# Performance work log

Hardware: AMD Instinct MI355X
Metric: run time of the kernel (lower is better)

## Reference

```python
import jax, jax.numpy as jnp
import numpy as np

N_NODES = 50000
N_EDGES = 640000
IN_CH = 128
OUT_CH = 128


def setup_inputs() -> dict:
    key = jax.random.key(0)
    k1, k2, k3, k4 = jax.random.split(key, 4)
    x = jax.random.normal(k1, (N_NODES, IN_CH), dtype=jnp.float32)
    edge_index = jax.random.randint(k2, (2, N_EDGES), 0, N_NODES, dtype=jnp.int32)
    # nn.Linear params: W [out, in], b [out]
    bound = 1.0 / np.sqrt(IN_CH)
    W = jax.random.uniform(k3, (OUT_CH, IN_CH), minval=-bound, maxval=bound, dtype=jnp.float32)
    b = jax.random.uniform(k4, (OUT_CH,), minval=-bound, maxval=bound, dtype=jnp.float32)
    return {"x": x, "edge_index": edge_index, "W": W, "b": b}


def reference(x, edge_index, W, b):
    row, col = edge_index[0], edge_index[1]
    num_nodes = x.shape[0]
    # degree of each destination node (clamped to >= 1)
    deg = jax.ops.segment_sum(jnp.ones(row.shape[0], dtype=x.dtype), row,
                              num_segments=num_nodes)
    deg = jnp.maximum(deg, 1.0)
    # gather neighbor features and scatter-add into destinations
    agg = jax.ops.segment_sum(x[col], row, num_segments=num_nodes)
    agg = agg / deg[:, None]
    # residual + linear
    return (x + agg) @ W.T + b
```

## Files before the change

### kernel.cpp

```cpp
#include <hip/hip_runtime.h>

#define N_NODES 50000
#define N_EDGES 640000
#define CH 128
#define NBINS 1563
#define NTILES 1563
#define FILLB 128
#define EPB 5000
#define OBW (NBINS + 1)
#define CAPR 48

typedef __bf16 bf16_t;
typedef bf16_t bf16x8 __attribute__((ext_vector_type(8)));
typedef float f32x4 __attribute__((ext_vector_type(4)));

__device__ __forceinline__ ushort f2bf(float f) {
  union { float f; unsigned u; } v; v.f = f;
  unsigned r = v.u + 0x7FFFu + ((v.u >> 16) & 1u);
  return (ushort)(r >> 16);
}
__device__ __forceinline__ float bflo(unsigned u) {
  union { unsigned u; float f; } v; v.u = u << 16; return v.f;
}
__device__ __forceinline__ float bfhi(unsigned u) {
  union { unsigned u; float f; } v; v.u = u & 0xFFFF0000u; return v.f;
}
__device__ __forceinline__ unsigned pack2(float lo, float hi) {
  return (unsigned)f2bf(lo) | ((unsigned)f2bf(hi) << 16);
}
__device__ __forceinline__ void addrow(float* acc, uint4 v) {
  acc[0] += bflo(v.x); acc[1] += bfhi(v.x);
  acc[2] += bflo(v.y); acc[3] += bfhi(v.y);
  acc[4] += bflo(v.z); acc[5] += bfhi(v.z);
  acc[6] += bflo(v.w); acc[7] += bfhi(v.w);
}


__global__ __launch_bounds__(256) void fill_conv(const int* __restrict__ row,
                                                 const int* __restrict__ col,
                                                 unsigned* __restrict__ binRec,
                                                 ushort* __restrict__ obo,
                                                 const float4* __restrict__ x4,
                                                 uint4* __restrict__ xb4,
                                                 const float4* __restrict__ W4,
                                                 uint4* __restrict__ Wb4) {
  __shared__ int cnt[NBINS];
  __shared__ int parts[256];
  __shared__ __align__(16) unsigned recbuf[EPB];
  int bid = blockIdx.x;
  int tid = threadIdx.x;
  if (bid < FILLB) {
    for (int i = tid; i < NBINS; i += 256) cnt[i] = 0;
    __syncthreads();
    int base = bid * EPB;
    int4 r4s[5], c4s[5];
    bool val[5];
#pragma unroll
    for (int b = 0; b < 5; ++b) {
      int idx4 = b * 1024 + tid * 4;
      val[b] = idx4 < EPB;
      if (val[b]) {
        r4s[b] = *(const int4*)(row + base + idx4);
        c4s[b] = *(const int4*)(col + base + idx4);
      }
    }
    unsigned pkv[20];
    unsigned colp[10];
#pragma unroll
    for (int b = 0; b < 5; ++b) {
      if (val[b]) {
        int rr[4] = {r4s[b].x, r4s[b].y, r4s[b].z, r4s[b].w};
        int cc[4] = {c4s[b].x, c4s[b].y, c4s[b].z, c4s[b].w};
#pragma unroll
        for (int j = 0; j < 4; ++j) {
          int bi = rr[j] >> 5;
          int rk = atomicAdd(&cnt[bi], 1);
          pkv[b * 4 + j] = ((unsigned)bi << 13) |
                           ((unsigned)(rr[j] & 31) << 8) | (unsigned)rk;
        }
        colp[b * 2]     = ((unsigned)cc[0] & 0xFFFFu) | ((unsigned)cc[1] << 16);
        colp[b * 2 + 1] = ((unsigned)cc[2] & 0xFFFFu) | ((unsigned)cc[3] << 16);
      } else {
#pragma unroll
        for (int j = 0; j < 4; ++j) pkv[b * 4 + j] = 0xFFFFFFFFu;
        colp[b * 2] = 0; colp[b * 2 + 1] = 0;
      }
    }
    __syncthreads();
    int c7[7];
    int s = 0;
#pragma unroll
    for (int k = 0; k < 7; ++k) {
      int i = tid * 7 + k;
      int c = (i < NBINS) ? cnt[i] : 0;
      c7[k] = c; s += c;
    }
    parts[tid] = s;
    __syncthreads();
    for (int off = 1; off < 256; off <<= 1) {
      int v = (tid >= off) ? parts[tid - off] : 0;
      __syncthreads();
      parts[tid] += v;
      __syncthreads();
    }
    int run = (tid > 0) ? parts[tid - 1] : 0;
    ushort* orow = obo + bid * OBW;
#pragma unroll
    for (int k = 0; k < 7; ++k) {
      int i = tid * 7 + k;
      if (i < NBINS) {
        orow[i] = (ushort)run;
        cnt[i] = run;
        run += c7[k];
      }
    }
    if (tid == 0) orow[NBINS] = (ushort)EPB;
    __syncthreads();
#pragma unroll
    for (int k = 0; k < 20; ++k) {
      unsigned p = pkv[k];
      if (p != 0xFFFFFFFFu) {
        int bi = (int)(p >> 13);
        int lr5 = (int)((p >> 8) & 31u);
        int rk = (int)(p & 255u);
        unsigned cw = (colp[k >> 1] >> ((k & 1) * 16)) & 0xFFFFu;
        recbuf[cnt[bi] + rk] = ((unsigned)lr5 << 16) | cw;
      }
    }
    __syncthreads();
    uint4* gb4 = (uint4*)(binRec + base);
    const uint4* rb4 = (const uint4*)recbuf;
    for (int j = tid; j < EPB / 4; j += 256) gb4[j] = rb4[j];
  } else if (bid < FILLB + 3125) {
    int i = (bid - FILLB) * 256 + tid;
    float4 a = x4[i * 2], b = x4[i * 2 + 1];
    uint4 o;
    o.x = pack2(a.x, a.y); o.y = pack2(a.z, a.w);
    o.z = pack2(b.x, b.y); o.w = pack2(b.z, b.w);
    xb4[i] = o;
  } else {
    for (int i = tid; i < 2048; i += 256) {
      float4 c = W4[i * 2], d = W4[i * 2 + 1];
      uint4 w;
      w.x = pack2(c.x, c.y); w.y = pack2(c.z, c.w);
      w.z = pack2(d.x, d.y); w.w = pack2(d.z, d.w);
      Wb4[i] = w;
    }
  }
}

__global__ __launch_bounds__(256) void fused(const uint4* __restrict__ xb4,
                                             const unsigned* __restrict__ binRec,
                                             const ushort* __restrict__ obo,
                                             const uint4* __restrict__ Wb4,
                                             const float4* __restrict__ bias4,
                                             float4* __restrict__ out4) {
  __shared__ ushort hT[32 * CH];
  __shared__ __align__(16) ushort colL[32 * CAPR];
  __shared__ int rowcnt[32];
  int tid = threadIdx.x;
  int g = blockIdx.x;
  int m0 = g * 32;

  if (tid < 32) rowcnt[tid] = 0;
  __syncthreads();
  {
    int i = tid >> 1, sub = tid & 1;
    const ushort* orow = obo + i * OBW + g;
    int o0 = orow[0], o1 = orow[1];
    const unsigned* rbase = binRec + i * EPB;
    for (int p = o0 + sub; p < o1; p += 2) {
      unsigned rec = __builtin_nontemporal_load(rbase + p);
      int lr = (int)(rec >> 16);
      int pp = atomicAdd(&rowcnt[lr], 1);
      if (pp < CAPR) colL[lr * CAPR + pp] = (ushort)(rec & 0xFFFFu);
    }
  }
  __syncthreads();

  int wv = tid >> 6;
  int lane = tid & 63;
  int q = lane & 15;
  int grp = lane >> 4;
#pragma unroll
  for (int t = 0; t < 2; ++t) {
    int r = wv * 8 + t * 4 + grp;
    int node = m0 + r;
    int deg = rowcnt[r];
    int degc = deg < CAPR ? deg : CAPR;
    const ushort* arow = colL + r * CAPR;
    int nc = node < N_NODES ? node : 0;
    uint4 xi = xb4[nc * 16 + q];
    float acc[8] = {0.f, 0.f, 0.f, 0.f, 0.f, 0.f, 0.f, 0.f};
    int e = 0;
    for (; e + 7 < degc; e += 8) {
      uint4 ids = *(const uint4*)(arow + e);
      int n0 = ids.x & 0xFFFF, n1 = ids.x >> 16;
      int n2 = ids.y & 0xFFFF, n3 = ids.y >> 16;
      int n4 = ids.z & 0xFFFF, n5 = ids.z >> 16;
      int n6 = ids.w & 0xFFFF, n7 = ids.w >> 16;
      uint4 v0 = xb4[n0 * 16 + q];
      uint4 v1 = xb4[n1 * 16 + q];
      uint4 v2 = xb4[n2 * 16 + q];
      uint4 v3 = xb4[n3 * 16 + q];
      uint4 v4 = xb4[n4 * 16 + q];
      uint4 v5 = xb4[n5 * 16 + q];
      uint4 v6 = xb4[n6 * 16 + q];
      uint4 v7 = xb4[n7 * 16 + q];
      addrow(acc, v0); addrow(acc, v1); addrow(acc, v2); addrow(acc, v3);
      addrow(acc, v4); addrow(acc, v5); addrow(acc, v6); addrow(acc, v7);
    }
    if (e + 3 < degc) {
      uint2 ids = *(const uint2*)(arow + e);
      int n0 = ids.x & 0xFFFF, n1 = ids.x >> 16;
      int n2 = ids.y & 0xFFFF, n3 = ids.y >> 16;
      uint4 v0 = xb4[n0 * 16 + q];
      uint4 v1 = xb4[n1 * 16 + q];
      uint4 v2 = xb4[n2 * 16 + q];
      uint4 v3 = xb4[n3 * 16 + q];
      addrow(acc, v0); addrow(acc, v1); addrow(acc, v2); addrow(acc, v3);
      e += 4;
    }
    for (; e < degc; ++e) {
      uint4 v = xb4[(int)arow[e] * 16 + q];
      addrow(acc, v);
    }
    uint4 o = make_uint4(0, 0, 0, 0);
    if (node < N_NODES) {
      float s = 1.0f / fmaxf((float)deg, 1.0f);
      o.x = pack2(bflo(xi.x) + acc[0] * s, bfhi(xi.x) + acc[1] * s);
      o.y = pack2(bflo(xi.y) + acc[2] * s, bfhi(xi.y) + acc[3] * s);
      o.z = pack2(bflo(xi.z) + acc[4] * s, bfhi(xi.z) + acc[5] * s);
      o.w = pack2(bflo(xi.w) + acc[6] * s, bfhi(xi.w) + acc[7] * s);
    }
    *(uint4*)&hT[r * CH + ((q ^ (r & 15)) << 3)] = o;
  }
  __syncthreads();

  int qq = grp;
  int mt = wv & 1;
  int nbase = (wv >> 1) * 4;
  const ushort* hbase = &hT[(mt * 16 + q) * CH];
  bf16x8 hb0 = *(const bf16x8*)(hbase + (((qq + 0) ^ q) << 3));
  bf16x8 hb1 = *(const bf16x8*)(hbase + (((qq + 4) ^ q) << 3));
  bf16x8 hb2 = *(const bf16x8*)(hbase + (((qq + 8) ^ q) << 3));
  bf16x8 hb3 = *(const bf16x8*)(hbase + (((qq + 12) ^ q) << 3));
  int m = m0 + mt * 16 + q;
#pragma unroll
  for (int i = 0; i < 4; ++i) {
    int nt = nbase + i;
    const uint4* wr = Wb4 + (nt * 16 + q) * 16 + qq;
    bf16x8 w0 = __builtin_bit_cast(bf16x8, wr[0]);
    bf16x8 w1 = __builtin_bit_cast(bf16x8, wr[4]);
    bf16x8 w2 = __builtin_bit_cast(bf16x8, wr[8]);
    bf16x8 w3 = __builtin_bit_cast(bf16x8, wr[12]);
    f32x4 acc = {0.f, 0.f, 0.f, 0.f};
    acc = __builtin_amdgcn_mfma_f32_16x16x32_bf16(w0, hb0, acc, 0, 0, 0);
    acc = __builtin_amdgcn_mfma_f32_16x16x32_bf16(w1, hb1, acc, 0, 0, 0);
    acc = __builtin_amdgcn_mfma_f32_16x16x32_bf16(w2, hb2, acc, 0, 0, 0);
    acc = __builtin_amdgcn_mfma_f32_16x16x32_bf16(w3, hb3, acc, 0, 0, 0);
    if (m < N_NODES) {
      float4 bv = bias4[nt * 4 + qq];
      f32x4 o;
      o.x = acc[0] + bv.x;
      o.y = acc[1] + bv.y;
      o.z = acc[2] + bv.z;
      o.w = acc[3] + bv.w;
      __builtin_nontemporal_store(o, (f32x4*)(out4 + (size_t)m * 32 + nt * 4 + qq));
    }
  }
}

extern "C" void kernel_launch(void* const* d_in, const int* in_sizes, int n_in,
                              void* d_out, int out_size, void* d_ws, size_t ws_size,
                              hipStream_t stream) {
  const float* x  = (const float*)d_in[0];
  const int*   ei = (const int*)d_in[1];
  const float* W  = (const float*)d_in[2];
  const float* bb = (const float*)d_in[3];

  char* ws = (char*)d_ws;
  unsigned* binRec = (unsigned*)ws;
  ushort*   obo    = (ushort*)(ws + 2560000);
  uint4*    Wb4    = (uint4*)(ws + 2960384);
  uint4*    xb4    = (uint4*)(ws + 2993152);

  fill_conv<<<FILLB + 3125 + 1, 256, 0, stream>>>(ei, ei + N_EDGES, binRec, obo,
                                                  (const float4*)x, xb4,
                                                  (const float4*)W, Wb4);
  fused<<<NTILES, 256, 0, stream>>>(xb4, binRec, obo, Wb4,
                                    (const float4*)bb, (float4*)d_out);
}
```

Baseline: 131.8 us.

## Split binning into 256 blocks with transposed offsets, widen fused kernel to 512 threads

```diff
diff --git a/kernel.cpp b/kernel.cpp
--- a/kernel.cpp
+++ b/kernel.cpp
@@ -5,9 +5,8 @@
 #define CH 128
 #define NBINS 1563
 #define NTILES 1563
-#define FILLB 128
-#define EPB 5000
-#define OBW (NBINS + 1)
+#define BINB 256
+#define EPB 2500
 #define CAPR 48
 
 typedef __bf16 bf16_t;
@@ -36,103 +35,105 @@
 }
 
 
-__global__ __launch_bounds__(256) void fill_conv(const int* __restrict__ row,
-                                                 const int* __restrict__ col,
-                                                 unsigned* __restrict__ binRec,
-                                                 ushort* __restrict__ obo,
-                                                 const float4* __restrict__ x4,
-                                                 uint4* __restrict__ xb4,
-                                                 const float4* __restrict__ W4,
-                                                 uint4* __restrict__ Wb4) {
+__global__ __launch_bounds__(256) void bink(const int* __restrict__ row,
+                                            const int* __restrict__ col,
+                                            unsigned* __restrict__ binRec,
+                                            ushort* __restrict__ obot) {
   __shared__ int cnt[NBINS];
   __shared__ int parts[256];
   __shared__ __align__(16) unsigned recbuf[EPB];
   int bid = blockIdx.x;
   int tid = threadIdx.x;
-  if (bid < FILLB) {
-    for (int i = tid; i < NBINS; i += 256) cnt[i] = 0;
+  for (int i = tid; i < NBINS; i += 256) cnt[i] = 0;
+  __syncthreads();
+  int base = bid * EPB;
+  int4 r4s[3], c4s[3];
+  bool val[3];
+#pragma unroll
+  for (int b = 0; b < 3; ++b) {
+    int idx4 = b * 1024 + tid * 4;
+    val[b] = idx4 < EPB;
+    if (val[b]) {
+      r4s[b] = *(const int4*)(row + base + idx4);
+      c4s[b] = *(const int4*)(col + base + idx4);
+    }
+  }
+  unsigned pkv[12];
+  unsigned colp[6];
+#pragma unroll
+  for (int b = 0; b < 3; ++b) {
+    if (val[b]) {
+      int rr[4] = {r4s[b].x, r4s[b].y, r4s[b].z, r4s[b].w};
+      int cc[4] = {c4s[b].x, c4s[b].y, c4s[b].z, c4s[b].w};
+#pragma unroll
+      for (int j = 0; j < 4; ++j) {
+        int bi = rr[j] >> 5;
+        int rk = atomicAdd(&cnt[bi], 1);
+        pkv[b * 4 + j] = ((unsigned)bi << 13) |
+                         ((unsigned)(rr[j] & 31) << 8) | (unsigned)rk;
+      }
+      colp[b * 2]     = ((unsigned)cc[0] & 0xFFFFu) | ((unsigned)cc[1] << 16);
+      colp[b * 2 + 1] = ((unsigned)cc[2] & 0xFFFFu) | ((unsigned)cc[3] << 16);
+    } else {
+#pragma unroll
+      for (int j = 0; j < 4; ++j) pkv[b * 4 + j] = 0xFFFFFFFFu;
+      colp[b * 2] = 0; colp[b * 2 + 1] = 0;
+    }
+  }
+  __syncthreads();
+  int c7[7];
+  int s = 0;
+#pragma unroll
+  for (int k = 0; k < 7; ++k) {
+    int i = tid * 7 + k;
+    int c = (i < NBINS) ? cnt[i] : 0;
+    c7[k] = c; s += c;
+  }
+  parts[tid] = s;
+  __syncthreads();
+  for (int off = 1; off < 256; off <<= 1) {
+    int v = (tid >= off) ? parts[tid - off] : 0;
     __syncthreads();
-    int base = bid * EPB;
-    int4 r4s[5], c4s[5];
-    bool val[5];
-#pragma unroll
-    for (int b = 0; b < 5; ++b) {
-      int idx4 = b * 1024 + tid * 4;
-      val[b] = idx4 < EPB;
-      if (val[b]) {
-        r4s[b] = *(const int4*)(row + base + idx4);
-        c4s[b] = *(const int4*)(col + base + idx4);
-      }
-    }
-    unsigned pkv[20];
-    unsigned colp[10];
-#pragma unroll
-    for (int b = 0; b < 5; ++b) {
-      if (val[b]) {
-        int rr[4] = {r4s[b].x, r4s[b].y, r4s[b].z, r4s[b].w};
-        int cc[4] = {c4s[b].x, c4s[b].y, c4s[b].z, c4s[b].w};
-#pragma unroll
-        for (int j = 0; j < 4; ++j) {
-          int bi = rr[j] >> 5;
-          int rk = atomicAdd(&cnt[bi], 1);
-          pkv[b * 4 + j] = ((unsigned)bi << 13) |
-                           ((unsigned)(rr[j] & 31) << 8) | (unsigned)rk;
-        }
-        colp[b * 2]     = ((unsigned)cc[0] & 0xFFFFu) | ((unsigned)cc[1] << 16);
-        colp[b * 2 + 1] = ((unsigned)cc[2] & 0xFFFFu) | ((unsigned)cc[3] << 16);
-      } else {
-#pragma unroll
-        for (int j = 0; j < 4; ++j) pkv[b * 4 + j] = 0xFFFFFFFFu;
-        colp[b * 2] = 0; colp[b * 2 + 1] = 0;
-      }
-    }
+    parts[tid] += v;
     __syncthreads();
-    int c7[7];
-    int s = 0;
-#pragma unroll
-    for (int k = 0; k < 7; ++k) {
-      int i = tid * 7 + k;
-      int c = (i < NBINS) ? cnt[i] : 0;
-      c7[k] = c; s += c;
-    }
-    parts[tid] = s;
-    __syncthreads();
-    for (int off = 1; off < 256; off <<= 1) {
-      int v = (tid >= off) ? parts[tid - off] : 0;
-      __syncthreads();
-      parts[tid] += v;
-      __syncthreads();
-    }
-    int run = (tid > 0) ? parts[tid - 1] : 0;
-    ushort* orow = obo + bid * OBW;
-#pragma unroll
-    for (int k = 0; k < 7; ++k) {
-      int i = tid * 7 + k;
-      if (i < NBINS) {
-        orow[i] = (ushort)run;
-        cnt[i] = run;
-        run += c7[k];
-      }
-    }
-    if (tid == 0) orow[NBINS] = (ushort)EPB;
-    __syncthreads();
-#pragma unroll
-    for (int k = 0; k < 20; ++k) {
-      unsigned p = pkv[k];
-      if (p != 0xFFFFFFFFu) {
-        int bi = (int)(p >> 13);
-        int lr5 = (int)((p >> 8) & 31u);
-        int rk = (int)(p & 255u);
-        unsigned cw = (colp[k >> 1] >> ((k & 1) * 16)) & 0xFFFFu;
-        recbuf[cnt[bi] + rk] = ((unsigned)lr5 << 16) | cw;
-      }
-    }
-    __syncthreads();
-    uint4* gb4 = (uint4*)(binRec + base);
-    const uint4* rb4 = (const uint4*)recbuf;
-    for (int j = tid; j < EPB / 4; j += 256) gb4[j] = rb4[j];
-  } else if (bid < FILLB + 3125) {
-    int i = (bid - FILLB) * 256 + tid;
+  }
+  int run = (tid > 0) ? parts[tid - 1] : 0;
+#pragma unroll
+  for (int k = 0; k < 7; ++k) {
+    int i = tid * 7 + k;
+    if (i < NBINS) {
+      obot[i * BINB + bid] = (ushort)run;
+      cnt[i] = run;
+      run += c7[k];
+    }
+  }
+  if (tid == 0) obot[NBINS * BINB + bid] = (ushort)EPB;
+  __syncthreads();
+#pragma unroll
+  for (int k = 0; k < 12; ++k) {
+    unsigned p = pkv[k];
+    if (p != 0xFFFFFFFFu) {
+      int bi = (int)(p >> 13);
+      int lr5 = (int)((p >> 8) & 31u);
+      int rk = (int)(p & 255u);
+      unsigned cw = (colp[k >> 1] >> ((k & 1) * 16)) & 0xFFFFu;
+      recbuf[cnt[bi] + rk] = ((unsigned)lr5 << 16) | cw;
+    }
+  }
+  __syncthreads();
+  uint4* gb4 = (uint4*)(binRec + base);
+  const uint4* rb4 = (const uint4*)recbuf;
+  for (int j = tid; j < EPB / 4; j += 256) gb4[j] = rb4[j];
+}
+
+__global__ __launch_bounds__(256) void conv(const float4* __restrict__ x4,
+                                            uint4* __restrict__ xb4,
+                                            const float4* __restrict__ W4,
+                                            uint4* __restrict__ Wb4) {
+  int bid = blockIdx.x;
+  int tid = threadIdx.x;
+  if (bid < 3125) {
+    int i = bid * 256 + tid;
     float4 a = x4[i * 2], b = x4[i * 2 + 1];
     uint4 o;
     o.x = pack2(a.x, a.y); o.y = pack2(a.z, a.w);
@@ -149,9 +150,9 @@
   }
 }
 
-__global__ __launch_bounds__(256) void fused(const uint4* __restrict__ xb4,
+__global__ __launch_bounds__(512) void fused(const uint4* __restrict__ xb4,
                                              const unsigned* __restrict__ binRec,
-                                             const ushort* __restrict__ obo,
+                                             const ushort* __restrict__ obot,
                                              const uint4* __restrict__ Wb4,
                                              const float4* __restrict__ bias4,
                                              float4* __restrict__ out4) {
@@ -166,11 +167,11 @@
   __syncthreads();
   {
     int i = tid >> 1, sub = tid & 1;
-    const ushort* orow = obo + i * OBW + g;
-    int o0 = orow[0], o1 = orow[1];
+    int o0 = obot[g * BINB + i];
+    int o1 = obot[(g + 1) * BINB + i];
     const unsigned* rbase = binRec + i * EPB;
     for (int p = o0 + sub; p < o1; p += 2) {
-      unsigned rec = __builtin_nontemporal_load(rbase + p);
+      unsigned rec = rbase[p];
       int lr = (int)(rec >> 16);
       int pp = atomicAdd(&rowcnt[lr], 1);
       if (pp < CAPR) colL[lr * CAPR + pp] = (ushort)(rec & 0xFFFFu);
@@ -182,64 +183,61 @@
   int lane = tid & 63;
   int q = lane & 15;
   int grp = lane >> 4;
-#pragma unroll
-  for (int t = 0; t < 2; ++t) {
-    int r = wv * 8 + t * 4 + grp;
-    int node = m0 + r;
-    int deg = rowcnt[r];
-    int degc = deg < CAPR ? deg : CAPR;
-    const ushort* arow = colL + r * CAPR;
-    int nc = node < N_NODES ? node : 0;
-    uint4 xi = xb4[nc * 16 + q];
-    float acc[8] = {0.f, 0.f, 0.f, 0.f, 0.f, 0.f, 0.f, 0.f};
-    int e = 0;
-    for (; e + 7 < degc; e += 8) {
-      uint4 ids = *(const uint4*)(arow + e);
-      int n0 = ids.x & 0xFFFF, n1 = ids.x >> 16;
-      int n2 = ids.y & 0xFFFF, n3 = ids.y >> 16;
-      int n4 = ids.z & 0xFFFF, n5 = ids.z >> 16;
-      int n6 = ids.w & 0xFFFF, n7 = ids.w >> 16;
-      uint4 v0 = xb4[n0 * 16 + q];
-      uint4 v1 = xb4[n1 * 16 + q];
-      uint4 v2 = xb4[n2 * 16 + q];
-      uint4 v3 = xb4[n3 * 16 + q];
-      uint4 v4 = xb4[n4 * 16 + q];
-      uint4 v5 = xb4[n5 * 16 + q];
-      uint4 v6 = xb4[n6 * 16 + q];
-      uint4 v7 = xb4[n7 * 16 + q];
-      addrow(acc, v0); addrow(acc, v1); addrow(acc, v2); addrow(acc, v3);
-      addrow(acc, v4); addrow(acc, v5); addrow(acc, v6); addrow(acc, v7);
-    }
-    if (e + 3 < degc) {
-      uint2 ids = *(const uint2*)(arow + e);
-      int n0 = ids.x & 0xFFFF, n1 = ids.x >> 16;
-      int n2 = ids.y & 0xFFFF, n3 = ids.y >> 16;
-      uint4 v0 = xb4[n0 * 16 + q];
-      uint4 v1 = xb4[n1 * 16 + q];
-      uint4 v2 = xb4[n2 * 16 + q];
-      uint4 v3 = xb4[n3 * 16 + q];
-      addrow(acc, v0); addrow(acc, v1); addrow(acc, v2); addrow(acc, v3);
-      e += 4;
-    }
-    for (; e < degc; ++e) {
-      uint4 v = xb4[(int)arow[e] * 16 + q];
-      addrow(acc, v);
-    }
-    uint4 o = make_uint4(0, 0, 0, 0);
-    if (node < N_NODES) {
-      float s = 1.0f / fmaxf((float)deg, 1.0f);
-      o.x = pack2(bflo(xi.x) + acc[0] * s, bfhi(xi.x) + acc[1] * s);
-      o.y = pack2(bflo(xi.y) + acc[2] * s, bfhi(xi.y) + acc[3] * s);
-      o.z = pack2(bflo(xi.z) + acc[4] * s, bfhi(xi.z) + acc[5] * s);
-      o.w = pack2(bflo(xi.w) + acc[6] * s, bfhi(xi.w) + acc[7] * s);
-    }
-    *(uint4*)&hT[r * CH + ((q ^ (r & 15)) << 3)] = o;
-  }
+  int r = wv * 4 + grp;
+  int node = m0 + r;
+  int deg = rowcnt[r];
+  int degc = deg < CAPR ? deg : CAPR;
+  const ushort* arow = colL + r * CAPR;
+  int nc = node < N_NODES ? node : 0;
+  uint4 xi = xb4[nc * 16 + q];
+  float acc[8] = {0.f, 0.f, 0.f, 0.f, 0.f, 0.f, 0.f, 0.f};
+  int e = 0;
+  for (; e + 7 < degc; e += 8) {
+    uint4 ids = *(const uint4*)(arow + e);
+    int n0 = ids.x & 0xFFFF, n1 = ids.x >> 16;
+    int n2 = ids.y & 0xFFFF, n3 = ids.y >> 16;
+    int n4 = ids.z & 0xFFFF, n5 = ids.z >> 16;
+    int n6 = ids.w & 0xFFFF, n7 = ids.w >> 16;
+    uint4 v0 = xb4[n0 * 16 + q];
+    uint4 v1 = xb4[n1 * 16 + q];
+    uint4 v2 = xb4[n2 * 16 + q];
+    uint4 v3 = xb4[n3 * 16 + q];
+    uint4 v4 = xb4[n4 * 16 + q];
+    uint4 v5 = xb4[n5 * 16 + q];
+    uint4 v6 = xb4[n6 * 16 + q];
+    uint4 v7 = xb4[n7 * 16 + q];
+    addrow(acc, v0); addrow(acc, v1); addrow(acc, v2); addrow(acc, v3);
+    addrow(acc, v4); addrow(acc, v5); addrow(acc, v6); addrow(acc, v7);
+  }
+  if (e + 3 < degc) {
+    uint2 ids = *(const uint2*)(arow + e);
+    int n0 = ids.x & 0xFFFF, n1 = ids.x >> 16;
+    int n2 = ids.y & 0xFFFF, n3 = ids.y >> 16;
+    uint4 v0 = xb4[n0 * 16 + q];
+    uint4 v1 = xb4[n1 * 16 + q];
+    uint4 v2 = xb4[n2 * 16 + q];
+    uint4 v3 = xb4[n3 * 16 + q];
+    addrow(acc, v0); addrow(acc, v1); addrow(acc, v2); addrow(acc, v3);
+    e += 4;
+  }
+  for (; e < degc; ++e) {
+    uint4 v = xb4[(int)arow[e] * 16 + q];
+    addrow(acc, v);
+  }
+  uint4 o = make_uint4(0, 0, 0, 0);
+  if (node < N_NODES) {
+    float s = 1.0f / fmaxf((float)deg, 1.0f);
+    o.x = pack2(bflo(xi.x) + acc[0] * s, bfhi(xi.x) + acc[1] * s);
+    o.y = pack2(bflo(xi.y) + acc[2] * s, bfhi(xi.y) + acc[3] * s);
+    o.z = pack2(bflo(xi.z) + acc[4] * s, bfhi(xi.z) + acc[5] * s);
+    o.w = pack2(bflo(xi.w) + acc[6] * s, bfhi(xi.w) + acc[7] * s);
+  }
+  *(uint4*)&hT[r * CH + ((q ^ (r & 15)) << 3)] = o;
   __syncthreads();
 
   int qq = grp;
   int mt = wv & 1;
-  int nbase = (wv >> 1) * 4;
+  int nbase = (wv >> 1) * 2;
   const ushort* hbase = &hT[(mt * 16 + q) * CH];
   bf16x8 hb0 = *(const bf16x8*)(hbase + (((qq + 0) ^ q) << 3));
   bf16x8 hb1 = *(const bf16x8*)(hbase + (((qq + 4) ^ q) << 3));
@@ -247,26 +245,26 @@
   bf16x8 hb3 = *(const bf16x8*)(hbase + (((qq + 12) ^ q) << 3));
   int m = m0 + mt * 16 + q;
 #pragma unroll
-  for (int i = 0; i < 4; ++i) {
+  for (int i = 0; i < 2; ++i) {
     int nt = nbase + i;
     const uint4* wr = Wb4 + (nt * 16 + q) * 16 + qq;
     bf16x8 w0 = __builtin_bit_cast(bf16x8, wr[0]);
     bf16x8 w1 = __builtin_bit_cast(bf16x8, wr[4]);
     bf16x8 w2 = __builtin_bit_cast(bf16x8, wr[8]);
     bf16x8 w3 = __builtin_bit_cast(bf16x8, wr[12]);
-    f32x4 acc = {0.f, 0.f, 0.f, 0.f};
-    acc = __builtin_amdgcn_mfma_f32_16x16x32_bf16(w0, hb0, acc, 0, 0, 0);
-    acc = __builtin_amdgcn_mfma_f32_16x16x32_bf16(w1, hb1, acc, 0, 0, 0);
-    acc = __builtin_amdgcn_mfma_f32_16x16x32_bf16(w2, hb2, acc, 0, 0, 0);
-    acc = __builtin_amdgcn_mfma_f32_16x16x32_bf16(w3, hb3, acc, 0, 0, 0);
+    f32x4 acc2 = {0.f, 0.f, 0.f, 0.f};
+    acc2 = __builtin_amdgcn_mfma_f32_16x16x32_bf16(w0, hb0, acc2, 0, 0, 0);
+    acc2 = __builtin_amdgcn_mfma_f32_16x16x32_bf16(w1, hb1, acc2, 0, 0, 0);
+    acc2 = __builtin_amdgcn_mfma_f32_16x16x32_bf16(w2, hb2, acc2, 0, 0, 0);
+    acc2 = __builtin_amdgcn_mfma_f32_16x16x32_bf16(w3, hb3, acc2, 0, 0, 0);
     if (m < N_NODES) {
       float4 bv = bias4[nt * 4 + qq];
-      f32x4 o;
-      o.x = acc[0] + bv.x;
-      o.y = acc[1] + bv.y;
-      o.z = acc[2] + bv.z;
-      o.w = acc[3] + bv.w;
-      __builtin_nontemporal_store(o, (f32x4*)(out4 + (size_t)m * 32 + nt * 4 + qq));
+      f32x4 ov;
+      ov.x = acc2[0] + bv.x;
+      ov.y = acc2[1] + bv.y;
+      ov.z = acc2[2] + bv.z;
+      ov.w = acc2[3] + bv.w;
+      __builtin_nontemporal_store(ov, (f32x4*)(out4 + (size_t)m * 32 + nt * 4 + qq));
     }
   }
 }
@@ -281,13 +279,12 @@
 
   char* ws = (char*)d_ws;
   unsigned* binRec = (unsigned*)ws;
-  ushort*   obo    = (ushort*)(ws + 2560000);
-  uint4*    Wb4    = (uint4*)(ws + 2960384);
-  uint4*    xb4    = (uint4*)(ws + 2993152);
-
-  fill_conv<<<FILLB + 3125 + 1, 256, 0, stream>>>(ei, ei + N_EDGES, binRec, obo,
-                                                  (const float4*)x, xb4,
-                                                  (const float4*)W, Wb4);
-  fused<<<NTILES, 256, 0, stream>>>(xb4, binRec, obo, Wb4,
+  ushort*   obot   = (ushort*)(ws + 2560000);
+  uint4*    Wb4    = (uint4*)(ws + 3360768);
+  uint4*    xb4    = (uint4*)(ws + 3393536);
+
+  bink<<<BINB, 256, 0, stream>>>(ei, ei + N_EDGES, binRec, obot);
+  conv<<<3126, 256, 0, stream>>>((const float4*)x, xb4, (const float4*)W, Wb4);
+  fused<<<NTILES, 512, 0, stream>>>(xb4, binRec, obot, Wb4,
                                     (const float4*)bb, (float4*)d_out);
 }
```

New measurement: 133.1 us. About the same (+1.0%).
